# Optimization experiments

Hardware: AMD Instinct MI355X
Metric: run time of the kernel (lower is better)

The kernel has to match this reference:

```python
import jax, jax.numpy as jnp
import numpy as np

BETA = 0.25  # commitment weight (legacy=True branch)


def setup_inputs() -> dict:
    key = jax.random.key(0)
    k1, k2 = jax.random.split(key)
    B, C, H, W = 32, 256, 32, 32
    N_E, E_DIM = 1024, 256
    z = jax.random.normal(k1, (B, C, H, W), dtype=jnp.float32)
    # original init: uniform(-1/n_e, 1/n_e)
    emb = jax.random.uniform(k2, (N_E, E_DIM), dtype=jnp.float32,
                             minval=-1.0 / N_E, maxval=1.0 / N_E)
    return {"z": z, "emb": emb}


def reference(z, emb):
    B, C, H, W = z.shape
    sg = jax.lax.stop_gradient
    zt = jnp.transpose(z, (0, 2, 3, 1))            # b h w c
    zf = zt.reshape(-1, C)                          # (N, e_dim)
    # ||z||^2 + ||e||^2 - 2 z e^T  -> (N, n_e)
    d = (jnp.sum(zf * zf, axis=1, keepdims=True)
         + jnp.sum(emb * emb, axis=1)
         - 2.0 * jnp.einsum('nd,kd->nk', zf, emb))
    idx = jnp.argmin(d, axis=1)                     # (N,)
    z_q = emb[idx].reshape(zt.shape)                # b h w c
    # legacy=True loss
    loss = (jnp.mean((sg(z_q) - zt) ** 2)
            + BETA * jnp.mean((z_q - sg(zt)) ** 2))
    # straight-through estimator
    z_q_st = zt + sg(z_q - zt)
    z_q_out = jnp.transpose(z_q_st, (0, 3, 1, 2))   # b c h w
    z_indices = idx.reshape(B, 1, H, W)
    return z_q_out, loss, z_indices
```

## Files before the change

### kernel.cpp

```cpp
#include <hip/hip_runtime.h>


#define WS_B 0
#define WS_A 1024
#define WS_PV 132096
#define WS_E1 656384
#define WS_E2 787456
#define WS_LIST 918528
#define WS_CNT 951296
#define WS_Z1T 951304
#define WS_FUSED_BYTES ((size_t)(WS_Z1T + 8388608) * 4)

#define DDIM 256
#define LOSS_OFF 8388608
#define IDX_OFF 8388609
#define Z2T_OFF 8388608
#define REFINE_THR 8e-5f

typedef __attribute__((ext_vector_type(8))) short bf16x8;
typedef __attribute__((ext_vector_type(4))) float f32x4;
typedef __attribute__((ext_vector_type(8))) ushort u16x8;

__device__ __forceinline__ ushort bf16_rne(float x) {
  unsigned u = __float_as_uint(x);
  return (ushort)((u + 0x7FFFu + ((u >> 16) & 1u)) >> 16);
}
__device__ __forceinline__ float bf16f(ushort h) {
  return __uint_as_float(((unsigned)h) << 16);
}
__device__ __forceinline__ void gld16(void* l, const void* g) {
  __builtin_amdgcn_global_load_lds(
      (const __attribute__((address_space(1))) unsigned int*)g,
      (__attribute__((address_space(3))) unsigned int*)l, 16, 0, 0);
}

__global__ __launch_bounds__(256) void k_prep(const float* __restrict__ z,
                                              const float* __restrict__ emb,
                                              ushort* __restrict__ zt,
                                              float* __restrict__ ws,
                                              float* __restrict__ out) {
  __shared__ float lt[64][132];
  __shared__ float sq[128];
  const int tid = threadIdx.x;
  if (blockIdx.x >= 1024) {
    const int k = (blockIdx.x - 1024) * 256 + tid;
    if (k == 0) { out[LOSS_OFF] = 0.0f; ((int*)ws)[WS_CNT] = 0; }
    const int ct = k >> 8, n = k & 255;
    const float* er = emb + k * DDIM;
    ushort* e1t = (ushort*)(ws + WS_E1);
    ushort* e2t = (ushort*)(ws + WS_E2);
    float bsum = 0.f;
    for (int s = 0; s < 8; ++s) {
#pragma unroll
      for (int kq = 0; kq < 4; ++kq) {
        const float4 v0 = *(const float4*)(er + s * 32 + kq * 8);
        const float4 v1 = *(const float4*)(er + s * 32 + kq * 8 + 4);
        const float v[8] = {v0.x, v0.y, v0.z, v0.w, v1.x, v1.y, v1.z, v1.w};
        u16x8 h, l;
#pragma unroll
        for (int j = 0; j < 8; ++j) {
          bsum = fmaf(v[j], v[j], bsum);
          h[j] = bf16_rne(v[j]);
          l[j] = bf16_rne(v[j] - bf16f(h[j]));
        }
        const int off = ct * 65536 + s * 8192 + kq * 2048 + n * 8;
        *(u16x8*)(e1t + off) = h;
        *(u16x8*)(e2t + off) = l;
      }
    }
    ws[WS_B + k] = bsum;
    return;
  }
  const int rt = blockIdx.x >> 2;
  const int qp = blockIdx.x & 3;
  const int b = rt >> 3;
  const int hw0 = (rt & 7) << 7;
  ushort* z1t = zt;
  ushort* z2t = zt + Z2T_OFF;
  const int m = tid & 127, half = tid >> 7;
  const int lc = tid >> 2, lq = tid & 3;
  float as[4] = {0.f, 0.f, 0.f, 0.f};
  {
    const float* src = z + b * 262144 + ((qp << 6) + lc) * 1024 + hw0 + (lq << 5);
#pragma unroll
    for (int i = 0; i < 8; ++i)
      *(float4*)&lt[lc][(lq << 5) + (i << 2)] = *(const float4*)(src + (i << 2));
    __syncthreads();
    const int s = (qp << 1) + half;
#pragma unroll
    for (int kq = 0; kq < 4; ++kq) {
      u16x8 h, l;
#pragma unroll
      for (int j = 0; j < 8; ++j) {
        const float v = lt[(half << 5) + (kq << 3) + j][m];
        as[j & 3] = fmaf(v, v, as[j & 3]);
        h[j] = bf16_rne(v);
        l[j] = bf16_rne(v - bf16f(h[j]));
      }
      const int off = rt * 32768 + ((s << 2) + kq) * 1024 + (m << 3);
      *(u16x8*)(z1t + off) = h;
      *(u16x8*)(z2t + off) = l;
    }
    __syncthreads();
  }
  const float asum = (as[0] + as[1]) + (as[2] + as[3]);
  if (half) sq[m] = asum;
  __syncthreads();
  if (!half) ws[WS_A + qp * 32768 + rt * 128 + m] = asum + sq[m];
}

__global__ __launch_bounds__(512, 2) void k_score(const ushort* __restrict__ zt,
                                                  const float* __restrict__ emb,
                                                  float* out,
                                                  float* __restrict__ ws,
                                                  int fused) {
  __shared__ __align__(16) ushort lds[2][24576];
  __shared__ float Bs[1024];
  __shared__ float pvs[2048];
  __shared__ float sm2[8];
  __shared__ int idxs[128];
  const int tid = threadIdx.x;
  const int rt = blockIdx.x;
  const int row0 = rt << 7;
  const ushort* z1t = zt;
  const ushort* z2t = zt + Z2T_OFF;
  const ushort* e1t = (const ushort*)(ws + WS_E1);
  const ushort* e2t = (const ushort*)(ws + WS_E2);
  const int w = tid >> 6, L = tid & 63;
  const int l15 = L & 15, kq = L >> 4;
  const int wr = w >> 2, wc = w & 3;

  Bs[tid] = ws[WS_B + tid];
  Bs[tid + 512] = ws[WS_B + tid + 512];
  float Av[4][4];
#pragma unroll
  for (int mi = 0; mi < 4; ++mi) {
    const int base = row0 + (wr << 6) + (mi << 4) + (kq << 2);
    const float4 a0 = *(const float4*)(ws + WS_A + base);
    const float4 a1 = *(const float4*)(ws + WS_A + 32768 + base);
    const float4 a2 = *(const float4*)(ws + WS_A + 65536 + base);
    const float4 a3 = *(const float4*)(ws + WS_A + 98304 + base);
    Av[mi][0] = (a0.x + a1.x) + (a2.x + a3.x);
    Av[mi][1] = (a0.y + a1.y) + (a2.y + a3.y);
    Av[mi][2] = (a0.z + a1.z) + (a2.z + a3.z);
    Av[mi][3] = (a0.w + a1.w) + (a2.w + a3.w);
  }
  asm volatile("s_waitcnt vmcnt(0)" ::: "memory");
  __builtin_amdgcn_sched_barrier(0);
  __syncthreads();

  const ushort* cbase[6];
  bool cisz[6];
#pragma unroll
  for (int c = 0; c < 6; ++c) {
    const int f = w * 6 + c;
    if (f < 8)       { cbase[c] = z1t + rt * 32768 + (f << 9) + (L << 3); cisz[c] = true; }
    else if (f < 16) { cbase[c] = z2t + rt * 32768 + ((f - 8) << 9) + (L << 3); cisz[c] = true; }
    else if (f < 32) { cbase[c] = e1t + ((f - 16) << 9) + (L << 3); cisz[c] = false; }
    else             { cbase[c] = e2t + ((f - 32) << 9) + (L << 3); cisz[c] = false; }
  }
  auto stage = [&](int q, int bf) {
    const int s = q & 7, ct = q >> 3;
    const int zoff = s << 12;
    const int eoff = (ct << 16) + (s << 13);
#pragma unroll
    for (int c = 0; c < 6; ++c) {
      const ushort* src = cbase[c] + (cisz[c] ? zoff : eoff);
      gld16(&lds[bf][(w * 6 + c) << 9], src);
    }
  };

  f32x4 acc[4][4];
  float v1[4][4], v2[4][4];
  int i1[4][4];
#pragma unroll
  for (int mi = 0; mi < 4; ++mi)
#pragma unroll
    for (int r = 0; r < 4; ++r) {
      acc[mi][r] = (f32x4){0.f, 0.f, 0.f, 0.f};
      v1[mi][r] = 3.0e38f; v2[mi][r] = 3.0e38f; i1[mi][r] = 0;
    }

  stage(0, 0);
  stage(1, 1);

  auto body = [&](int q, int cur, bool last) {
    if (!last) asm volatile("s_waitcnt vmcnt(6)" ::: "memory");
    else       asm volatile("s_waitcnt vmcnt(0)" ::: "memory");
    __builtin_amdgcn_sched_barrier(0);
    __builtin_amdgcn_s_barrier();
    __builtin_amdgcn_sched_barrier(0);
    const ushort* lb = lds[cur];
    bf16x8 a1[4], a2[4], b1[4], b2[4];
#pragma unroll
    for (int mi = 0; mi < 4; ++mi) {
      const int off = (kq << 10) + (((wr << 6) + (mi << 4) + l15) << 3);
      a1[mi] = *(const bf16x8*)&lb[off];
      a2[mi] = *(const bf16x8*)&lb[4096 + off];
    }
#pragma unroll
    for (int nj = 0; nj < 4; ++nj) {
      const int off = (kq << 11) + (((wc << 6) + (nj << 4) + l15) << 3);
      b1[nj] = *(const bf16x8*)&lb[8192 + off];
      b2[nj] = *(const bf16x8*)&lb[16384 + off];
    }
    asm volatile("s_waitcnt lgkmcnt(0)" ::: "memory");
    __builtin_amdgcn_sched_barrier(0);
    __builtin_amdgcn_s_barrier();
    __builtin_amdgcn_sched_barrier(0);
    if (q < 30) stage(q + 2, cur);
    __builtin_amdgcn_s_setprio(1);
#pragma unroll
    for (int mi = 0; mi < 4; ++mi)
#pragma unroll
      for (int nj = 0; nj < 4; ++nj) {
        acc[mi][nj] = __builtin_amdgcn_mfma_f32_16x16x32_bf16(a2[mi], b1[nj], acc[mi][nj], 0, 0, 0);
        acc[mi][nj] = __builtin_amdgcn_mfma_f32_16x16x32_bf16(a1[mi], b2[nj], acc[mi][nj], 0, 0, 0);
        acc[mi][nj] = __builtin_amdgcn_mfma_f32_16x16x32_bf16(a1[mi], b1[nj], acc[mi][nj], 0, 0, 0);
      }
    __builtin_amdgcn_s_setprio(0);
    if ((q & 7) == 7) {
      const int ct = q >> 3;
      float bb[4];
#pragma unroll
      for (int nj = 0; nj < 4; ++nj)
        bb[nj] = Bs[(ct << 8) + (wc << 6) + (nj << 4) + l15];
      float cm[4][4];
#pragma unroll
      for (int mi = 0; mi < 4; ++mi)
#pragma unroll
        for (int r = 0; r < 4; ++r) cm[mi][r] = 3.0e38f;
#pragma unroll
      for (int mi = 0; mi < 4; ++mi)
#pragma unroll
        for (int nj = 0; nj < 4; ++nj) {
          const int kg = (ct << 8) + (wc << 6) + (nj << 4) + l15;
#pragma unroll
          for (int r = 0; r < 4; ++r) {
            const float sc = fmaf(-2.0f, acc[mi][nj][r], Av[mi][r] + bb[nj]);
            if (sc < v1[mi][r]) { v2[mi][r] = v1[mi][r]; v1[mi][r] = sc; i1[mi][r] = kg; }
            else if (sc < v2[mi][r]) v2[mi][r] = sc;
            cm[mi][r] = fminf(cm[mi][r], sc);
          }
          acc[mi][nj] = (f32x4){0.f, 0.f, 0.f, 0.f};
        }
#pragma unroll
      for (int mi = 0; mi < 4; ++mi)
#pragma unroll
        for (int r = 0; r < 4; ++r) {
          float cv = cm[mi][r];
#pragma unroll
          for (int o = 1; o < 16; o <<= 1) cv = fminf(cv, __shfl_xor(cv, o));
          if (l15 == 0) {
            const int rowl = (wr << 6) + (mi << 4) + (kq << 2) + r;
            pvs[((ct << 2) | wc) * 128 + rowl] = cv;
          }
        }
    }
  };

  for (int q = 0; q < 31; ++q) body(q, q & 1, false);
  body(31, 1, true);

#pragma unroll
  for (int mi = 0; mi < 4; ++mi)
#pragma unroll
    for (int r = 0; r < 4; ++r) {
      float a = v1[mi][r], bb = v2[mi][r];
      int ii = i1[mi][r];
#pragma unroll
      for (int o = 1; o < 16; o <<= 1) {
        const float oa = __shfl_xor(a, o);
        const float ob = __shfl_xor(bb, o);
        const int oi = __shfl_xor(ii, o);
        bb = fminf(fminf(bb, ob), fmaxf(a, oa));
        if (oa < a || (oa == a && oi < ii)) { a = oa; ii = oi; }
      }
      v1[mi][r] = a; v2[mi][r] = bb; i1[mi][r] = ii;
    }

  __syncthreads();
  for (int i = tid; i < 2048; i += 512) {
    const int c = i >> 7, rl = i & 127;
    ws[WS_PV + (c << 15) + row0 + rl] = pvs[i];
  }
  float* red = (float*)&lds[0][0];
  if (l15 == 0) {
#pragma unroll
    for (int mi = 0; mi < 4; ++mi)
#pragma unroll
      for (int r = 0; r < 4; ++r) {
        const int rl = (wr << 6) + (mi << 4) + (kq << 2) + r;
        const int b3 = (wc * 128 + rl) * 3;
        red[b3] = v1[mi][r];
        red[b3 + 1] = v2[mi][r];
        red[b3 + 2] = (float)i1[mi][r];
      }
  }
  __syncthreads();
  float losss = 0.f;
  if (tid < 128) {
    float fv1 = 3.0e38f, fv2 = 3.0e38f;
    int fi = 0;
#pragma unroll
    for (int c = 0; c < 4; ++c) {
      const int b3 = (c * 128 + tid) * 3;
      const float a1 = red[b3], a2 = red[b3 + 1];
      const int ai = (int)red[b3 + 2];
      if (a1 < fv1 || (a1 == fv1 && ai < fi)) { fv2 = fminf(fv1, a2); fv1 = a1; fi = ai; }
      else fv2 = fminf(fv2, a1);
    }
    const int row = row0 + tid;
    out[IDX_OFF + row] = (float)fi;
    idxs[tid] = fi;
    if (fv2 - fv1 < REFINE_THR) {
      const int slot = atomicAdd((int*)ws + WS_CNT, 1);
      ((int*)ws)[WS_LIST + slot] = row;
    }
    losss = fv1;
  }
#pragma unroll
  for (int o = 32; o; o >>= 1) losss += __shfl_down(losss, o);
  if ((tid & 63) == 0) sm2[tid >> 6] = losss;
  __syncthreads();
  if (tid == 0) {
    float t = 0.f;
#pragma unroll
    for (int i = 0; i < 8; ++i) t += sm2[i];
    atomicAdd(out + LOSS_OFF, t * (1.25f / 8388608.0f));
  }

  if (fused) {
    float* lt2 = (float*)&lds[0][0];
    const int b = rt >> 3;
    const int hw0 = (rt & 7) << 7;
    for (int ph = 0; ph < 2; ++ph) {
      __syncthreads();
      {
        const int r = tid >> 3, seg = tid & 7;
        const float* er = emb + idxs[(ph << 6) + r] * DDIM;
        float* dst = lt2 + r * 257;
#pragma unroll
        for (int i = 0; i < 8; ++i) {
          const int c = (seg << 2) + (i << 5);
          const float4 v = *(const float4*)(er + c);
          dst[c] = v.x; dst[c + 1] = v.y; dst[c + 2] = v.z; dst[c + 3] = v.w;
        }
      }
      __syncthreads();
      {
        const int c = tid >> 1;
        const int r0 = (tid & 1) << 5;
        float* dsto = out + b * 262144 + c * 1024 + hw0 + (ph << 6) + r0;
#pragma unroll
        for (int i = 0; i < 32; i += 4) {
          float4 v;
          v.x = lt2[(r0 + i + 0) * 257 + c];
          v.y = lt2[(r0 + i + 1) * 257 + c];
          v.z = lt2[(r0 + i + 2) * 257 + c];
          v.w = lt2[(r0 + i + 3) * 257 + c];
          *(float4*)(dsto + i) = v;
        }
      }
    }
  }
}

__global__ __launch_bounds__(256) void k_refine(const float* __restrict__ z,
                                                const float* __restrict__ emb,
                                                const float* __restrict__ ws,
                                                float* __restrict__ out,
                                                int fused) {
  __shared__ float zs[4][256];
  const int tid = threadIdx.x;
  const int w = tid >> 6, L = tid & 63;
  const int wg = blockIdx.x * 4 + w;
  const int cnt = ((const int*)ws)[WS_CNT];
  for (int e = wg; e < cnt; e += 1024) {
    const int row = ((const int*)ws)[WS_LIST + e];
    const int b = row >> 10, hw = row & 1023;
#pragma unroll
    for (int q = 0; q < 4; ++q)
      zs[w][(q << 6) + L] = z[b * 262144 + (((q << 6) + L) << 10) + hw];
    asm volatile("s_waitcnt lgkmcnt(0)" ::: "memory");
    float v1c = (L < 16) ? ws[WS_PV + (L << 15) + row] : 3.0e38f;
    float v1 = v1c;
#pragma unroll
    for (int o = 1; o < 64; o <<= 1) v1 = fminf(v1, __shfl_xor(v1, o));
    const float A = (ws[WS_A + row] + ws[WS_A + 32768 + row]) +
                    (ws[WS_A + 65536 + row] + ws[WS_A + 98304 + row]);
    float bv = 3.0e38f;
    int bk = 0;
    for (int tc = 0; tc < 16; ++tc) {
      const float bc = __shfl(v1c, tc);
      if (bc <= v1 + REFINE_THR) {
        const int k = (tc << 6) + L;
        const float* er = emb + k * DDIM;
        float s = 0.f;
        for (int d = 0; d < DDIM; ++d) s = fmaf(zs[w][d], er[d], s);
        const float sc = fmaf(-2.0f, s, A + ws[WS_B + k]);
        if (sc < bv) { bv = sc; bk = k; }
      }
    }
#pragma unroll
    for (int o = 1; o < 64; o <<= 1) {
      const float ov = __shfl_xor(bv, o);
      const int ok = __shfl_xor(bk, o);
      if (ov < bv || (ov == bv && ok < bk)) { bv = ov; bk = ok; }
    }
    if (L == 0) out[IDX_OFF + row] = (float)bk;
    if (fused) {
#pragma unroll
      for (int ci = 0; ci < 4; ++ci) {
        const int c = (ci << 6) + L;
        out[b * 262144 + c * 1024 + hw] = emb[bk * DDIM + c];
      }
    }
  }
}

__global__ __launch_bounds__(256) void k_gather(const float* __restrict__ emb,
                                                float* __restrict__ out) {
  const int tid = threadIdx.x;
  const int e0 = (blockIdx.x * 256 + tid) * 16;
  const int b = e0 >> 18;
  const int c = (e0 >> 10) & 255;
  const int n0 = (b << 10) + (e0 & 1023);
#pragma unroll
  for (int g = 0; g < 4; ++g) {
    float q[4];
#pragma unroll
    for (int j = 0; j < 4; ++j) {
      const int id = (int)(out[IDX_OFF + n0 + g * 4 + j] + 0.5f);
      q[j] = emb[id * DDIM + c];
    }
    const float4 qv = {q[0], q[1], q[2], q[3]};
    *(float4*)(out + e0 + g * 4) = qv;
  }
}

extern "C" void kernel_launch(void* const* d_in, const int* in_sizes, int n_in,
                              void* d_out, int out_size, void* d_ws, size_t ws_size,
                              hipStream_t stream) {
  const float* z = (const float*)d_in[0];
  const float* emb = (const float*)d_in[1];
  float* out = (float*)d_out;
  float* ws = (float*)d_ws;
  const int fused = (ws_size >= WS_FUSED_BYTES) ? 1 : 0;
  ushort* zt = fused ? (ushort*)(ws + WS_Z1T) : (ushort*)out;

  k_prep<<<1028, 256, 0, stream>>>(z, emb, zt, ws, out);
  k_score<<<256, 512, 0, stream>>>(zt, emb, out, ws, fused);
  k_refine<<<256, 256, 0, stream>>>(z, emb, ws, out, fused);
  if (!fused) k_gather<<<2048, 256, 0, stream>>>(emb, out);
}
```

Measured before the change: 135.9 us.

## Halve score tile rows and load codebook fragments directly from global memory

The score kernel now processes 64 rows per block instead of 128 and launches twice as many blocks. Only the z tiles are staged through LDS; codebook bf16 fragments are read straight from global (L2-resident) into registers each step. The LDS footprint drops sharply and the launch bound is raised to allow four blocks per CU, aiming for more occupancy and parallelism across the 256 CUs. The cost is twice as many global reads of the codebook per row, with those global load latencies now exposed inside the MFMA loop.

Result: faster. 123.6 us (-9.1%).

```diff
diff --git a/kernel.cpp b/kernel.cpp
--- a/kernel.cpp
+++ b/kernel.cpp
@@ -109,19 +109,22 @@
   if (!half) ws[WS_A + qp * 32768 + rt * 128 + m] = asum + sq[m];
 }
 
-__global__ __launch_bounds__(512, 2) void k_score(const ushort* __restrict__ zt,
+__global__ __launch_bounds__(512, 4) void k_score(const ushort* __restrict__ zt,
                                                   const float* __restrict__ emb,
                                                   float* out,
                                                   float* __restrict__ ws,
                                                   int fused) {
-  __shared__ __align__(16) ushort lds[2][24576];
-  __shared__ float Bs[1024];
-  __shared__ float pvs[2048];
-  __shared__ float sm2[8];
-  __shared__ int idxs[128];
+  __shared__ __align__(16) char smem[33312];
+  ushort* zl = (ushort*)smem;
+  float* Bs = (float*)(smem + 16384);
+  float* pvs = (float*)(smem + 20480);
+  float* sm2 = (float*)(smem + 33024);
+  int* idxs = (int*)(smem + 33056);
   const int tid = threadIdx.x;
-  const int rt = blockIdx.x;
-  const int row0 = rt << 7;
+  const int bid = blockIdx.x;
+  const int rt = ((bid >> 4) << 3) | (bid & 7);
+  const int mh = ((bid >> 3) & 1) << 6;
+  const int row0 = (rt << 7) + mh;
   const ushort* z1t = zt;
   const ushort* z2t = zt + Z2T_OFF;
   const ushort* e1t = (const ushort*)(ws + WS_E1);
@@ -132,10 +135,10 @@
 
   Bs[tid] = ws[WS_B + tid];
   Bs[tid + 512] = ws[WS_B + tid + 512];
-  float Av[4][4];
-#pragma unroll
-  for (int mi = 0; mi < 4; ++mi) {
-    const int base = row0 + (wr << 6) + (mi << 4) + (kq << 2);
+  float Av[2][4];
+#pragma unroll
+  for (int mi = 0; mi < 2; ++mi) {
+    const int base = row0 + (wr << 5) + (mi << 4) + (kq << 2);
     const float4 a0 = *(const float4*)(ws + WS_A + base);
     const float4 a1 = *(const float4*)(ws + WS_A + 32768 + base);
     const float4 a2 = *(const float4*)(ws + WS_A + 65536 + base);
@@ -149,32 +152,19 @@
   __builtin_amdgcn_sched_barrier(0);
   __syncthreads();
 
-  const ushort* cbase[6];
-  bool cisz[6];
-#pragma unroll
-  for (int c = 0; c < 6; ++c) {
-    const int f = w * 6 + c;
-    if (f < 8)       { cbase[c] = z1t + rt * 32768 + (f << 9) + (L << 3); cisz[c] = true; }
-    else if (f < 16) { cbase[c] = z2t + rt * 32768 + ((f - 8) << 9) + (L << 3); cisz[c] = true; }
-    else if (f < 32) { cbase[c] = e1t + ((f - 16) << 9) + (L << 3); cisz[c] = false; }
-    else             { cbase[c] = e2t + ((f - 32) << 9) + (L << 3); cisz[c] = false; }
-  }
+  const ushort* zsrc = (w < 4 ? z1t : z2t) + rt * 32768 + ((w & 3) << 10)
+                       + (mh << 3) + (L << 3);
+  ushort* zdst0 = zl + ((w & 3) << 9) + ((w >> 2) << 11);
   auto stage = [&](int q, int bf) {
-    const int s = q & 7, ct = q >> 3;
-    const int zoff = s << 12;
-    const int eoff = (ct << 16) + (s << 13);
-#pragma unroll
-    for (int c = 0; c < 6; ++c) {
-      const ushort* src = cbase[c] + (cisz[c] ? zoff : eoff);
-      gld16(&lds[bf][(w * 6 + c) << 9], src);
-    }
+    gld16(zdst0 + (bf << 12), zsrc + ((q & 7) << 12));
   };
-
-  f32x4 acc[4][4];
-  float v1[4][4], v2[4][4];
-  int i1[4][4];
-#pragma unroll
-  for (int mi = 0; mi < 4; ++mi)
+  const int ebase_th = (kq << 11) + (((wc << 6) + l15) << 3);
+
+  f32x4 acc[2][4];
+  float v1[2][4], v2[2][4];
+  int i1[2][4];
+#pragma unroll
+  for (int mi = 0; mi < 2; ++mi)
 #pragma unroll
     for (int r = 0; r < 4; ++r) {
       acc[mi][r] = (f32x4){0.f, 0.f, 0.f, 0.f};
@@ -185,33 +175,37 @@
   stage(1, 1);
 
   auto body = [&](int q, int cur, bool last) {
-    if (!last) asm volatile("s_waitcnt vmcnt(6)" ::: "memory");
+    if (!last) asm volatile("s_waitcnt vmcnt(1)" ::: "memory");
     else       asm volatile("s_waitcnt vmcnt(0)" ::: "memory");
     __builtin_amdgcn_sched_barrier(0);
     __builtin_amdgcn_s_barrier();
     __builtin_amdgcn_sched_barrier(0);
-    const ushort* lb = lds[cur];
-    bf16x8 a1[4], a2[4], b1[4], b2[4];
-#pragma unroll
-    for (int mi = 0; mi < 4; ++mi) {
-      const int off = (kq << 10) + (((wr << 6) + (mi << 4) + l15) << 3);
+    const ushort* lb = zl + (cur << 12);
+    bf16x8 a1[2], a2[2], b1[4], b2[4];
+#pragma unroll
+    for (int mi = 0; mi < 2; ++mi) {
+      const int off = (kq << 9) + (((wr << 5) + (mi << 4) + l15) << 3);
       a1[mi] = *(const bf16x8*)&lb[off];
-      a2[mi] = *(const bf16x8*)&lb[4096 + off];
-    }
-#pragma unroll
-    for (int nj = 0; nj < 4; ++nj) {
-      const int off = (kq << 11) + (((wc << 6) + (nj << 4) + l15) << 3);
-      b1[nj] = *(const bf16x8*)&lb[8192 + off];
-      b2[nj] = *(const bf16x8*)&lb[16384 + off];
+      a2[mi] = *(const bf16x8*)&lb[2048 + off];
     }
     asm volatile("s_waitcnt lgkmcnt(0)" ::: "memory");
     __builtin_amdgcn_sched_barrier(0);
     __builtin_amdgcn_s_barrier();
     __builtin_amdgcn_sched_barrier(0);
+    {
+      const int ct = q >> 3, s = q & 7;
+      const ushort* e1p = e1t + (ct << 16) + (s << 13) + ebase_th;
+      const ushort* e2p = e2t + (ct << 16) + (s << 13) + ebase_th;
+#pragma unroll
+      for (int nj = 0; nj < 4; ++nj) {
+        b1[nj] = *(const bf16x8*)(e1p + (nj << 7));
+        b2[nj] = *(const bf16x8*)(e2p + (nj << 7));
+      }
+    }
     if (q < 30) stage(q + 2, cur);
     __builtin_amdgcn_s_setprio(1);
 #pragma unroll
-    for (int mi = 0; mi < 4; ++mi)
+    for (int mi = 0; mi < 2; ++mi)
 #pragma unroll
       for (int nj = 0; nj < 4; ++nj) {
         acc[mi][nj] = __builtin_amdgcn_mfma_f32_16x16x32_bf16(a2[mi], b1[nj], acc[mi][nj], 0, 0, 0);
@@ -225,13 +219,13 @@
 #pragma unroll
       for (int nj = 0; nj < 4; ++nj)
         bb[nj] = Bs[(ct << 8) + (wc << 6) + (nj << 4) + l15];
-      float cm[4][4];
-#pragma unroll
-      for (int mi = 0; mi < 4; ++mi)
+      float cm[2][4];
+#pragma unroll
+      for (int mi = 0; mi < 2; ++mi)
 #pragma unroll
         for (int r = 0; r < 4; ++r) cm[mi][r] = 3.0e38f;
 #pragma unroll
-      for (int mi = 0; mi < 4; ++mi)
+      for (int mi = 0; mi < 2; ++mi)
 #pragma unroll
         for (int nj = 0; nj < 4; ++nj) {
           const int kg = (ct << 8) + (wc << 6) + (nj << 4) + l15;
@@ -245,15 +239,15 @@
           acc[mi][nj] = (f32x4){0.f, 0.f, 0.f, 0.f};
         }
 #pragma unroll
-      for (int mi = 0; mi < 4; ++mi)
+      for (int mi = 0; mi < 2; ++mi)
 #pragma unroll
         for (int r = 0; r < 4; ++r) {
           float cv = cm[mi][r];
 #pragma unroll
           for (int o = 1; o < 16; o <<= 1) cv = fminf(cv, __shfl_xor(cv, o));
           if (l15 == 0) {
-            const int rowl = (wr << 6) + (mi << 4) + (kq << 2) + r;
-            pvs[((ct << 2) | wc) * 128 + rowl] = cv;
+            const int rowl = (wr << 5) + (mi << 4) + (kq << 2) + r;
+            pvs[((ct << 2) | wc) * 64 + rowl] = cv;
           }
         }
     }
@@ -263,7 +257,7 @@
   body(31, 1, true);
 
 #pragma unroll
-  for (int mi = 0; mi < 4; ++mi)
+  for (int mi = 0; mi < 2; ++mi)
 #pragma unroll
     for (int r = 0; r < 4; ++r) {
       float a = v1[mi][r], bb = v2[mi][r];
@@ -280,18 +274,18 @@
     }
 
   __syncthreads();
-  for (int i = tid; i < 2048; i += 512) {
-    const int c = i >> 7, rl = i & 127;
+  for (int i = tid; i < 1024; i += 512) {
+    const int c = i >> 6, rl = i & 63;
     ws[WS_PV + (c << 15) + row0 + rl] = pvs[i];
   }
-  float* red = (float*)&lds[0][0];
+  float* red = (float*)smem;
   if (l15 == 0) {
 #pragma unroll
-    for (int mi = 0; mi < 4; ++mi)
+    for (int mi = 0; mi < 2; ++mi)
 #pragma unroll
       for (int r = 0; r < 4; ++r) {
-        const int rl = (wr << 6) + (mi << 4) + (kq << 2) + r;
-        const int b3 = (wc * 128 + rl) * 3;
+        const int rl = (wr << 5) + (mi << 4) + (kq << 2) + r;
+        const int b3 = (wc * 64 + rl) * 3;
         red[b3] = v1[mi][r];
         red[b3 + 1] = v2[mi][r];
         red[b3 + 2] = (float)i1[mi][r];
@@ -299,12 +293,12 @@
   }
   __syncthreads();
   float losss = 0.f;
-  if (tid < 128) {
+  if (tid < 64) {
     float fv1 = 3.0e38f, fv2 = 3.0e38f;
     int fi = 0;
 #pragma unroll
     for (int c = 0; c < 4; ++c) {
-      const int b3 = (c * 128 + tid) * 3;
+      const int b3 = (c * 64 + tid) * 3;
       const float a1 = red[b3], a2 = red[b3 + 1];
       const int ai = (int)red[b3 + 2];
       if (a1 < fv1 || (a1 == fv1 && ai < fi)) { fv2 = fminf(fv1, a2); fv1 = a1; fi = ai; }
@@ -331,17 +325,17 @@
   }
 
   if (fused) {
-    float* lt2 = (float*)&lds[0][0];
-    const int b = rt >> 3;
-    const int hw0 = (rt & 7) << 7;
-    for (int ph = 0; ph < 2; ++ph) {
+    float* lt2 = (float*)smem;
+    const int b = row0 >> 10;
+    const int hw0 = row0 & 1023;
+    for (int ch = 0; ch < 2; ++ch) {
       __syncthreads();
       {
         const int r = tid >> 3, seg = tid & 7;
-        const float* er = emb + idxs[(ph << 6) + r] * DDIM;
-        float* dst = lt2 + r * 257;
-#pragma unroll
-        for (int i = 0; i < 8; ++i) {
+        const float* er = emb + idxs[r] * DDIM + (ch << 7);
+        float* dst = lt2 + r * 129;
+#pragma unroll
+        for (int i = 0; i < 4; ++i) {
           const int c = (seg << 2) + (i << 5);
           const float4 v = *(const float4*)(er + c);
           dst[c] = v.x; dst[c + 1] = v.y; dst[c + 2] = v.z; dst[c + 3] = v.w;
@@ -349,16 +343,16 @@
       }
       __syncthreads();
       {
-        const int c = tid >> 1;
-        const int r0 = (tid & 1) << 5;
-        float* dsto = out + b * 262144 + c * 1024 + hw0 + (ph << 6) + r0;
-#pragma unroll
-        for (int i = 0; i < 32; i += 4) {
+        const int c = tid >> 2;
+        const int r0 = (tid & 3) << 4;
+        float* dsto = out + b * 262144 + ((ch << 7) + c) * 1024 + hw0 + r0;
+#pragma unroll
+        for (int i = 0; i < 16; i += 4) {
           float4 v;
-          v.x = lt2[(r0 + i + 0) * 257 + c];
-          v.y = lt2[(r0 + i + 1) * 257 + c];
-          v.z = lt2[(r0 + i + 2) * 257 + c];
-          v.w = lt2[(r0 + i + 3) * 257 + c];
+          v.x = lt2[(r0 + i + 0) * 129 + c];
+          v.y = lt2[(r0 + i + 1) * 129 + c];
+          v.z = lt2[(r0 + i + 2) * 129 + c];
+          v.w = lt2[(r0 + i + 3) * 129 + c];
           *(float4*)(dsto + i) = v;
         }
       }
@@ -450,7 +444,7 @@
   ushort* zt = fused ? (ushort*)(ws + WS_Z1T) : (ushort*)out;
 
   k_prep<<<1028, 256, 0, stream>>>(z, emb, zt, ws, out);
-  k_score<<<256, 512, 0, stream>>>(zt, emb, out, ws, fused);
+  k_score<<<512, 512, 0, stream>>>(zt, emb, out, ws, fused);
   k_refine<<<256, 256, 0, stream>>>(z, emb, ws, out, fused);
   if (!fused) k_gather<<<2048, 256, 0, stream>>>(emb, out);
 }
```
